# Optimization experiments

Measured on AMD Instinct MI355X. Metric: run time of the kernel, lower is better.

Reference implementation:

```python
import jax, jax.numpy as jnp
import numpy as np

N_DRUG = 572
D = 512
K = 64          # neighbor_sample_size
T = 30000       # tail entities
R = 200         # relations
MAX_DEG = 32    # padded invariant_adj neighbor count
EPS = 1e-5


def setup_inputs() -> dict:
    key = jax.random.key(0)
    ks = jax.random.split(key, 10)
    return {
        "drug_embed_W": jax.random.normal(ks[0], (N_DRUG, D), jnp.float32),
        "rela_embed_W": jax.random.normal(ks[1], (R, D), jnp.float32),
        "ent_embed_W": jax.random.normal(ks[2], (T, D), jnp.float32),
        "Wa": jax.random.normal(ks[3], (D, D), jnp.float32) / np.float32(np.sqrt(D)),
        "lin_W": jax.random.normal(ks[4], (2 * D, D), jnp.float32) / np.float32(np.sqrt(2 * D)),
        "lin_b": jnp.zeros((D,), jnp.float32),
        "gamma": jnp.ones((D,), jnp.float32),
        "beta": jnp.zeros((D,), jnp.float32),
        "drug_name": jnp.arange(N_DRUG, dtype=jnp.int64 if jax.config.jax_enable_x64 else jnp.int32),
        "adj_tail": jax.random.randint(ks[5], (N_DRUG, K), 0, T),
        "adj_relation": jax.random.randint(ks[6], (N_DRUG, K), 0, R),
        "nbr_idx": jax.random.randint(ks[7], (N_DRUG, MAX_DEG), 0, N_DRUG),
        "nbr_deg": jax.random.randint(ks[8], (N_DRUG,), 0, MAX_DEG),
        "epoch": 2,
    }


def _forward(drug_embed_W, rela_embed_W, ent_embed_W, Wa, lin_W, lin_b, gamma, beta,
             drug_name, adj_tail, adj_relation, nbr_idx, nbr_deg, epoch):
    drug_e = drug_embed_W[drug_name]          # [N, D]
    rela = rela_embed_W[adj_relation]         # [N, K, D]
    ent = ent_embed_W[adj_tail]               # [N, K, D]

    # relation-aware attention over sampled neighbors (AttentionLayer)
    q = drug_e @ Wa                           # [N, D]
    scores = jnp.einsum('nd,nkd->nk', q, rela) * (1.0 / np.float32(np.sqrt(D)))
    attn = jax.nn.softmax(scores, axis=1)     # [N, K]
    agg = jnp.einsum('nk,nkd->nd', attn, ent) # [N, D]

    # Linear1: Linear(2D->D) + ReLU + BatchNorm1d (training-mode batch stats)
    h = jnp.concatenate([agg, drug_e], axis=1) @ lin_W + lin_b
    h = jax.nn.relu(h)
    mean = jnp.mean(h, axis=0)
    var = jnp.var(h, axis=0)                  # biased, as torch BN normalization
    drug_f = (h - mean) * jax.lax.rsqrt(var + EPS) * gamma + beta

    if epoch > 1:
        # sequential per-node neighbor-mean smoothing (in-place semantics)
        mask = (jnp.arange(MAX_DEG)[None, :] < nbr_deg[:, None])  # [N, MAX_DEG]

        def step(f, i):
            pos = nbr_idx[i]
            m = mask[i][:, None].astype(f.dtype)
            s = jnp.sum(f[pos] * m, axis=0)
            deg = nbr_deg[i]
            avg = s / jnp.maximum(deg, 1).astype(f.dtype)
            new = jnp.where(deg > 0, (avg + f[i]) * 0.5, f[i])
            return f.at[i].set(new), None

        drug_f, _ = jax.lax.scan(step, drug_f, jnp.arange(N_DRUG))
    return drug_f


def reference(drug_embed_W, rela_embed_W, ent_embed_W, Wa, lin_W, lin_b, gamma, beta,
              drug_name, adj_tail, adj_relation, nbr_idx, nbr_deg, epoch):
    return _forward(drug_embed_W, rela_embed_W, ent_embed_W, Wa, lin_W, lin_b, gamma, beta,
                    drug_name, adj_tail, adj_relation, nbr_idx, nbr_deg, epoch)
```

## Files before the change

kernel.cpp:

```cpp
#include <hip/hip_runtime.h>

#define N_DRUG 572
#define DIM 512
#define MAXDEG 32
#define FS 3

__global__ __launch_bounds__(256) void prep_kernel(
    const float* __restrict__ Wa, const float* __restrict__ relaW,
    const float* __restrict__ linW, float* __restrict__ linP,
    float* __restrict__ relaP)
{
    const int b = blockIdx.x;
    const int t = threadIdx.x;
    if (b < 512) {
        const int g = b * 256 + t;
        const int c = g & 511, k4 = g >> 9;
        const float4 v = make_float4(linW[(size_t)(k4 * 4 + 0) * 512 + c],
                                     linW[(size_t)(k4 * 4 + 1) * 512 + c],
                                     linW[(size_t)(k4 * 4 + 2) * 512 + c],
                                     linW[(size_t)(k4 * 4 + 3) * 512 + c]);
        *(float4*)&linP[((size_t)(c >> 6) * 256 + k4) * 256 + (c & 63) * 4] = v;
        return;
    }
    const int bb = b - 512;
    const int rb = bb >> 5, kb = bb & 31;
    const int wv = t >> 6, l = t & 63;
    const int r0 = rb * 16 + wv * 4;
    const int k0 = kb * 16;

    float a[4][8];
    #pragma unroll
    for (int rr = 0; rr < 4; ++rr) {
        const float4* ap = (const float4*)(relaW + (size_t)min(r0 + rr, 199) * 512 + l * 8);
        const float4 x = ap[0], y = ap[1];
        a[rr][0] = x.x; a[rr][1] = x.y; a[rr][2] = x.z; a[rr][3] = x.w;
        a[rr][4] = y.x; a[rr][5] = y.y; a[rr][6] = y.z; a[rr][7] = y.w;
    }
    float acc[64];
    #pragma unroll
    for (int i = 0; i < 64; ++i) acc[i] = 0.f;
    #pragma unroll
    for (int kk = 0; kk < 16; ++kk) {
        const float4* bp = (const float4*)(Wa + (size_t)(k0 + kk) * 512 + l * 8);
        const float4 x = bp[0], y = bp[1];
        const float bv[8] = {x.x, x.y, x.z, x.w, y.x, y.y, y.z, y.w};
        #pragma unroll
        for (int rr = 0; rr < 4; ++rr) {
            float s = acc[rr * 16 + kk];
            #pragma unroll
            for (int j = 0; j < 8; ++j) s = fmaf(a[rr][j], bv[j], s);
            acc[rr * 16 + kk] = s;
        }
    }
    #pragma unroll
    for (int off = 1; off <= 32; off <<= 1) {
        #pragma unroll
        for (int i = 0; i < 64; ++i) acc[i] += __shfl_xor(acc[i], off, 64);
    }
    float outv = acc[0];
    #pragma unroll
    for (int i = 1; i < 64; ++i) outv = (l == i) ? acc[i] : outv;
    const int rr = l >> 4, kk = l & 15;
    if (r0 + rr < 200) relaP[(size_t)(r0 + rr) * 512 + k0 + kk] = outv;
}

__global__ __launch_bounds__(256) void attn_kernel(
    const float* __restrict__ drugW, const float* __restrict__ relaP,
    const float* __restrict__ entW, const int* __restrict__ dn,
    const int* __restrict__ adj_tail, const int* __restrict__ adj_rel,
    float* __restrict__ cat)
{
    __shared__ float at[64];
    __shared__ int tails[64];
    __shared__ int rels[64];
    const int d = blockIdx.x;
    const int t = threadIdx.x;
    const int w = t >> 6, lane = t & 63;

    if (t < 64) {
        tails[t] = adj_tail[d * 64 + t];
        rels[t]  = adj_rel[d * 64 + t];
    }
    const int rd = dn[d];
    float qv[8];
    {
        const float4* qp = (const float4*)(drugW + (size_t)rd * 512 + lane * 8);
        const float4 x = qp[0], y = qp[1];
        qv[0] = x.x; qv[1] = x.y; qv[2] = x.z; qv[3] = x.w;
        qv[4] = y.x; qv[5] = y.y; qv[6] = y.z; qv[7] = y.w;
    }
    __syncthreads();

    #pragma unroll 4
    for (int kk = 0; kk < 16; ++kk) {
        const int k = w * 16 + kk;
        const float4* p = (const float4*)(relaP + (size_t)rels[k] * 512 + lane * 8);
        const float4 x = p[0], y = p[1];
        float s = 0.f;
        s = fmaf(qv[0], x.x, s); s = fmaf(qv[1], x.y, s);
        s = fmaf(qv[2], x.z, s); s = fmaf(qv[3], x.w, s);
        s = fmaf(qv[4], y.x, s); s = fmaf(qv[5], y.y, s);
        s = fmaf(qv[6], y.z, s); s = fmaf(qv[7], y.w, s);
        #pragma unroll
        for (int off = 32; off >= 1; off >>= 1) s += __shfl_xor(s, off, 64);
        if (lane == 0) at[k] = s * 0.0441941738241592f;
    }
    __syncthreads();

    if (w == 0) {
        const float s = at[lane];
        float m = s;
        #pragma unroll
        for (int off = 32; off >= 1; off >>= 1) m = fmaxf(m, __shfl_xor(m, off, 64));
        const float e = __expf(s - m);
        float sum = e;
        #pragma unroll
        for (int off = 32; off >= 1; off >>= 1) sum += __shfl_xor(sum, off, 64);
        at[lane] = e / sum;
    }
    __syncthreads();

    {
        const int c2 = t * 2;
        float a0 = 0.f, a1 = 0.f;
        #pragma unroll 8
        for (int k = 0; k < 64; ++k) {
            const float ak = at[k];
            const float2 e = *(const float2*)(entW + (size_t)tails[k] * 512 + c2);
            a0 = fmaf(ak, e.x, a0);
            a1 = fmaf(ak, e.y, a1);
        }
        float* o = cat + (size_t)d * 1024;
        *(float2*)&o[c2] = make_float2(a0, a1);
        const float2 de = *(const float2*)(drugW + (size_t)rd * 512 + c2);
        *(float2*)&o[512 + c2] = de;
    }
}

__global__ __launch_bounds__(512) void gemm_h(
    const float* __restrict__ A, const float* __restrict__ linP,
    const float* __restrict__ bias, float* __restrict__ out)
{
    __shared__ float red[8][8][128];
    const int t = threadIdx.x;
    const int wv = t >> 6, lane = t & 63;
    const int r0 = blockIdx.x * 8;
    const int half = lane >> 5;
    const int cw = (lane * 2) & 63;

    const float* wp = linP + ((size_t)(blockIdx.y * 2 + half) * 256 + wv * 32) * 256
                    + cw * 4;
    const float* ap[8];
    #pragma unroll
    for (int r = 0; r < 8; ++r)
        ap[r] = A + (size_t)min(r0 + r, N_DRUG - 1) * 1024 + wv * 128;

    float acc0[8] = {0.f, 0.f, 0.f, 0.f, 0.f, 0.f, 0.f, 0.f};
    float acc1[8] = {0.f, 0.f, 0.f, 0.f, 0.f, 0.f, 0.f, 0.f};
    #pragma unroll 2
    for (int k4 = 0; k4 < 32; ++k4) {
        const float4 w0 = *(const float4*)(wp + (size_t)k4 * 256);
        const float4 w1 = *(const float4*)(wp + (size_t)k4 * 256 + 4);
        #pragma unroll
        for (int r = 0; r < 8; ++r) {
            const float4 a = *(const float4*)(ap[r] + k4 * 4);
            acc0[r] = fmaf(a.x, w0.x, acc0[r]);
            acc0[r] = fmaf(a.y, w0.y, acc0[r]);
            acc0[r] = fmaf(a.z, w0.z, acc0[r]);
            acc0[r] = fmaf(a.w, w0.w, acc0[r]);
            acc1[r] = fmaf(a.x, w1.x, acc1[r]);
            acc1[r] = fmaf(a.y, w1.y, acc1[r]);
            acc1[r] = fmaf(a.z, w1.z, acc1[r]);
            acc1[r] = fmaf(a.w, w1.w, acc1[r]);
        }
    }
    #pragma unroll
    for (int r = 0; r < 8; ++r)
        *(float2*)&red[wv][r][lane * 2] = make_float2(acc0[r], acc1[r]);
    __syncthreads();

    #pragma unroll
    for (int u = 0; u < 2; ++u) {
        const int o = u * 512 + t;
        const int r = o >> 7, cc = o & 127;
        if (r0 + r < N_DRUG) {
            float v = red[0][r][cc];
            #pragma unroll
            for (int w = 1; w < 8; ++w) v += red[w][r][cc];
            v += bias[blockIdx.y * 128 + cc];
            out[(size_t)(r0 + r) * 512 + blockIdx.y * 128 + cc] = fmaxf(v, 0.f);
        }
    }
}

__global__ __launch_bounds__(64) void scan_kernel(
    float* hout, const float* __restrict__ gamma, const float* __restrict__ beta,
    const int* __restrict__ nbr_idx, const int* __restrict__ nbr_deg,
    const int* __restrict__ epoch)
{
    __shared__ float fs[(N_DRUG + 1) * FS];
    __shared__ alignas(16) unsigned short offs[N_DRUG * MAXDEG];
    __shared__ float2 ivw[N_DRUG];
    __shared__ int   mxs[N_DRUG];

    const int lane = threadIdx.x;
    const int col  = lane & 1;
    const int rg   = lane >> 1;
    const int c0   = blockIdx.x * 2;

    for (int i = lane; i < N_DRUG; i += 64) {
        const int d = nbr_deg[i];
        ivw[i] = (d > 0) ? make_float2(0.5f / (float)d, 0.5f) : make_float2(0.f, 1.f);
        const int4* np = (const int4*)&nbr_idx[i * MAXDEG];
        uint2* op = (uint2*)&offs[i * MAXDEG];
        int mx = -1;
        #pragma unroll
        for (int u = 0; u < 8; ++u) {
            int4 qq = np[u];
            const int b = u * 4;
            qq.x = (b + 0 < d) ? qq.x : N_DRUG;
            qq.y = (b + 1 < d) ? qq.y : N_DRUG;
            qq.z = (b + 2 < d) ? qq.z : N_DRUG;
            qq.w = (b + 3 < d) ? qq.w : N_DRUG;
            mx = max(mx, (qq.x < i) ? qq.x : -1);
            mx = max(mx, (qq.y < i) ? qq.y : -1);
            mx = max(mx, (qq.z < i) ? qq.z : -1);
            mx = max(mx, (qq.w < i) ? qq.w : -1);
            op[u] = make_uint2((unsigned)(qq.x * FS) | ((unsigned)(qq.y * FS) << 16),
                               (unsigned)(qq.z * FS) | ((unsigned)(qq.w * FS) << 16));
        }
        mxs[i] = mx;
    }

    float sl = 0.f, ql = 0.f;
    for (int r = rg; r < N_DRUG; r += 32) {
        const float v = hout[(size_t)r * DIM + c0 + col];
        fs[r * FS + col] = v;
        sl += v;
        ql = fmaf(v, v, ql);
    }
    if (lane < FS) fs[N_DRUG * FS + lane] = 0.f;
    #pragma unroll
    for (int off = 2; off <= 32; off <<= 1) {
        sl += __shfl_xor(sl, off, 64);
        ql += __shfl_xor(ql, off, 64);
    }
    const float mean = sl * (1.f / N_DRUG);
    const float var  = ql * (1.f / N_DRUG) - mean * mean;
    const float rstd = rsqrtf(var + 1e-5f);
    const float scl  = gamma[c0 + col] * rstd;
    const float shf  = beta[c0 + col] - mean * scl;

    for (int r = rg; r < N_DRUG; r += 32)
        fs[r * FS + col] = fmaf(fs[r * FS + col], scl, shf);

    if (epoch[0] > 1) {
        const int j  = lane >> 2;
        const int hh = (lane >> 1) & 1;
        const int cl = lane & 1;

        int gs = 0;
        int ge;
        {
            const int jj = 1 + lane;
            const bool flag = (lane >= 15) || (jj >= N_DRUG) ||
                              (mxs[min(jj, N_DRUG - 1)] >= 0);
            ge = 1 + (int)__builtin_ctzll(__ballot(flag) & 0xFFFFULL);
        }
        uint4 ca, cb;
        {
            const uint4* p = (const uint4*)&offs[j * MAXDEG + hh * 16];
            ca = p[0]; cb = p[1];
        }
        while (gs < N_DRUG) {
            const bool pred = (gs + j) < ge;
            float s0 = 0.f, s1 = 0.f;
#define G2(W) { s0 += fs[(W & 0xffffu) + cl]; s1 += fs[(W >> 16) + cl]; }
            if (pred) { G2(ca.x) G2(ca.y) G2(ca.z) G2(ca.w)
                        G2(cb.x) G2(cb.y) G2(cb.z) G2(cb.w) }
#undef G2
            uint4 na, nb;
            {
                const uint4* p = (const uint4*)&offs[min(ge + j, N_DRUG - 1) * MAXDEG + hh * 16];
                na = p[0]; nb = p[1];
            }
            int genext;
            {
                const int jj = ge + 1 + lane;
                const bool flag = (lane >= 15) || (jj >= N_DRUG) ||
                                  (mxs[min(jj, N_DRUG - 1)] >= ge);
                genext = ge + 1 + (int)__builtin_ctzll(__ballot(flag) & 0xFFFFULL);
            }
            float nv = 0.f;
            if (pred) {
                const float cur = fs[(gs + j) * FS + cl];
                const float2 iw = ivw[gs + j];
                float sh = s0 + s1;
                sh += __shfl_xor(sh, 2, 64);
                nv = fmaf(sh, iw.x, cur * iw.y);
            }
            asm volatile("" ::: "memory");
            if (pred && hh == 0) fs[(gs + j) * FS + cl] = nv;
            asm volatile("" ::: "memory");
            gs = ge;
            ge = genext;
            ca = na; cb = nb;
        }
    }

    for (int r = rg; r < N_DRUG; r += 32)
        hout[(size_t)r * DIM + c0 + col] = fs[r * FS + col];
}

extern "C" void kernel_launch(void* const* d_in, const int* in_sizes, int n_in,
                              void* d_out, int out_size, void* d_ws, size_t ws_size,
                              hipStream_t stream)
{
    const float* drugW = (const float*)d_in[0];
    const float* relaW = (const float*)d_in[1];
    const float* entW  = (const float*)d_in[2];
    const float* Wa    = (const float*)d_in[3];
    const float* linW  = (const float*)d_in[4];
    const float* linb  = (const float*)d_in[5];
    const float* gamma = (const float*)d_in[6];
    const float* beta  = (const float*)d_in[7];
    const int* drug_name = (const int*)d_in[8];
    const int* adj_tail  = (const int*)d_in[9];
    const int* adj_rel   = (const int*)d_in[10];
    const int* nbr_idx   = (const int*)d_in[11];
    const int* nbr_deg   = (const int*)d_in[12];
    const int* epoch     = (const int*)d_in[13];

    float* out = (float*)d_out;

    float* linP  = (float*)d_ws;
    float* relaP = (float*)((char*)d_ws + 2097152);
    float* cat   = (float*)((char*)d_ws + 2506752);

    prep_kernel<<<928, 256, 0, stream>>>(Wa, relaW, linW, linP, relaP);
    attn_kernel<<<N_DRUG, 256, 0, stream>>>(drugW, relaP, entW, drug_name,
                                            adj_tail, adj_rel, cat);
    gemm_h<<<dim3(72, 4), 512, 0, stream>>>(cat, linP, linb, out);
    scan_kernel<<<256, 64, 0, stream>>>(out, gamma, beta, nbr_idx, nbr_deg, epoch);
}
```

Before: 232.2 us.

## Precompute wavefront schedule once in prep kernel and prefetch scan state

The dependency-group schedule for the sequential neighbor smoothing is now computed once by an extra block of the prep kernel and written to workspace. Previously each of the 256 scan blocks recomputed it with a ballot on the serial critical path. The scan loop now reads the next group boundaries from shared memory, prefetches the next row's current value and weights, and replaces the cross-lane shuffle with a DPP move. Byte-offset tables are duplicated per column to drop an add from address computation, at the cost of extra shared memory.

```diff
diff --git a/kernel.cpp b/kernel.cpp
--- a/kernel.cpp
+++ b/kernel.cpp
@@ -3,12 +3,13 @@
 #define N_DRUG 572
 #define DIM 512
 #define MAXDEG 32
-#define FS 3
+#define FSB 12
 
 __global__ __launch_bounds__(256) void prep_kernel(
     const float* __restrict__ Wa, const float* __restrict__ relaW,
-    const float* __restrict__ linW, float* __restrict__ linP,
-    float* __restrict__ relaP)
+    const float* __restrict__ linW, const int* __restrict__ nbr_idx,
+    const int* __restrict__ nbr_deg, float* __restrict__ linP,
+    float* __restrict__ relaP, int* __restrict__ sched_g)
 {
     const int b = blockIdx.x;
     const int t = threadIdx.x;
@@ -22,6 +23,44 @@
         *(float4*)&linP[((size_t)(c >> 6) * 256 + k4) * 256 + (c & 63) * 4] = v;
         return;
     }
+    if (b == 928) {
+        __shared__ int mxs2[N_DRUG];
+        for (int i = t; i < N_DRUG; i += 256) {
+            const int d = nbr_deg[i];
+            const int4* np = (const int4*)&nbr_idx[i * MAXDEG];
+            int mx = -1;
+            #pragma unroll
+            for (int u = 0; u < 8; ++u) {
+                const int4 qq = np[u];
+                const int bb = u * 4;
+                mx = max(mx, (bb + 0 < d && qq.x < i) ? qq.x : -1);
+                mx = max(mx, (bb + 1 < d && qq.y < i) ? qq.y : -1);
+                mx = max(mx, (bb + 2 < d && qq.z < i) ? qq.z : -1);
+                mx = max(mx, (bb + 3 < d && qq.w < i) ? qq.w : -1);
+            }
+            mxs2[i] = mx;
+        }
+        __syncthreads();
+        if (t < 64) {
+            int gs = 0, nr = 0;
+            if (t == 0) sched_g[0] = 0;
+            while (gs < N_DRUG) {
+                const int jj = gs + 1 + t;
+                const bool flag = (t >= 15) || (jj >= N_DRUG) ||
+                                  (mxs2[min(jj, N_DRUG - 1)] >= gs);
+                const int ge = gs + 1 + (int)__builtin_ctzll(__ballot(flag) & 0xFFFFULL);
+                ++nr;
+                if (t == 0) sched_g[nr] = ge;
+                gs = ge;
+            }
+            if (t == 0) {
+                sched_g[nr + 1] = N_DRUG;
+                sched_g[nr + 2] = N_DRUG;
+                sched_g[nr + 3] = N_DRUG;
+            }
+        }
+        return;
+    }
     const int bb = b - 512;
     const int rb = bb >> 5, kb = bb & 31;
     const int wv = t >> 6, l = t & 63;
@@ -196,50 +235,51 @@
 __global__ __launch_bounds__(64) void scan_kernel(
     float* hout, const float* __restrict__ gamma, const float* __restrict__ beta,
     const int* __restrict__ nbr_idx, const int* __restrict__ nbr_deg,
-    const int* __restrict__ epoch)
-{
-    __shared__ float fs[(N_DRUG + 1) * FS];
-    __shared__ alignas(16) unsigned short offs[N_DRUG * MAXDEG];
+    const int* __restrict__ epoch, const int* __restrict__ sched_g)
+{
+    __shared__ alignas(16) unsigned char fsb[(N_DRUG + 1) * FSB];
+    __shared__ alignas(16) unsigned short offsA[N_DRUG * MAXDEG];
+    __shared__ alignas(16) unsigned short offsB[N_DRUG * MAXDEG];
     __shared__ float2 ivw[N_DRUG];
-    __shared__ int   mxs[N_DRUG];
+    __shared__ int sched[N_DRUG + 8];
 
     const int lane = threadIdx.x;
     const int col  = lane & 1;
     const int rg   = lane >> 1;
     const int c0   = blockIdx.x * 2;
+    const int cl4  = col * 4;
+
+    for (int i = lane; i < N_DRUG + 8; i += 64) sched[i] = sched_g[i];
 
     for (int i = lane; i < N_DRUG; i += 64) {
         const int d = nbr_deg[i];
         ivw[i] = (d > 0) ? make_float2(0.5f / (float)d, 0.5f) : make_float2(0.f, 1.f);
         const int4* np = (const int4*)&nbr_idx[i * MAXDEG];
-        uint2* op = (uint2*)&offs[i * MAXDEG];
-        int mx = -1;
+        uint2* opA = (uint2*)&offsA[i * MAXDEG];
+        uint2* opB = (uint2*)&offsB[i * MAXDEG];
         #pragma unroll
         for (int u = 0; u < 8; ++u) {
-            int4 qq = np[u];
+            const int4 qq = np[u];
             const int b = u * 4;
-            qq.x = (b + 0 < d) ? qq.x : N_DRUG;
-            qq.y = (b + 1 < d) ? qq.y : N_DRUG;
-            qq.z = (b + 2 < d) ? qq.z : N_DRUG;
-            qq.w = (b + 3 < d) ? qq.w : N_DRUG;
-            mx = max(mx, (qq.x < i) ? qq.x : -1);
-            mx = max(mx, (qq.y < i) ? qq.y : -1);
-            mx = max(mx, (qq.z < i) ? qq.z : -1);
-            mx = max(mx, (qq.w < i) ? qq.w : -1);
-            op[u] = make_uint2((unsigned)(qq.x * FS) | ((unsigned)(qq.y * FS) << 16),
-                               (unsigned)(qq.z * FS) | ((unsigned)(qq.w * FS) << 16));
-        }
-        mxs[i] = mx;
+            const int rx = (b + 0 < d) ? qq.x : N_DRUG;
+            const int ry = (b + 1 < d) ? qq.y : N_DRUG;
+            const int rz = (b + 2 < d) ? qq.z : N_DRUG;
+            const int rw = (b + 3 < d) ? qq.w : N_DRUG;
+            const unsigned w0 = (unsigned)(rx * FSB) | ((unsigned)(ry * FSB) << 16);
+            const unsigned w1 = (unsigned)(rz * FSB) | ((unsigned)(rw * FSB) << 16);
+            opA[u] = make_uint2(w0, w1);
+            opB[u] = make_uint2(w0 + 0x00040004u, w1 + 0x00040004u);
+        }
     }
 
     float sl = 0.f, ql = 0.f;
     for (int r = rg; r < N_DRUG; r += 32) {
         const float v = hout[(size_t)r * DIM + c0 + col];
-        fs[r * FS + col] = v;
+        *(float*)(fsb + r * FSB + cl4) = v;
         sl += v;
         ql = fmaf(v, v, ql);
     }
-    if (lane < FS) fs[N_DRUG * FS + lane] = 0.f;
+    if (lane < 3) *(float*)(fsb + N_DRUG * FSB + lane * 4) = 0.f;
     #pragma unroll
     for (int off = 2; off <= 32; off <<= 1) {
         sl += __shfl_xor(sl, off, 64);
@@ -251,65 +291,64 @@
     const float scl  = gamma[c0 + col] * rstd;
     const float shf  = beta[c0 + col] - mean * scl;
 
-    for (int r = rg; r < N_DRUG; r += 32)
-        fs[r * FS + col] = fmaf(fs[r * FS + col], scl, shf);
+    for (int r = rg; r < N_DRUG; r += 32) {
+        float* p = (float*)(fsb + r * FSB + cl4);
+        *p = fmaf(*p, scl, shf);
+    }
 
     if (epoch[0] > 1) {
         const int j  = lane >> 2;
         const int hh = (lane >> 1) & 1;
-        const int cl = lane & 1;
-
-        int gs = 0;
-        int ge;
-        {
-            const int jj = 1 + lane;
-            const bool flag = (lane >= 15) || (jj >= N_DRUG) ||
-                              (mxs[min(jj, N_DRUG - 1)] >= 0);
-            ge = 1 + (int)__builtin_ctzll(__ballot(flag) & 0xFFFFULL);
-        }
+        const unsigned short* obase = col ? offsB : offsA;
+
+        int gs  = 0;
+        int ge  = sched[1];
+        int ge2 = sched[2];
+        int rp  = 3;
         uint4 ca, cb;
         {
-            const uint4* p = (const uint4*)&offs[j * MAXDEG + hh * 16];
+            const uint4* p = (const uint4*)&obase[j * MAXDEG + hh * 16];
             ca = p[0]; cb = p[1];
         }
+        float  cur = *(const float*)(fsb + j * FSB + cl4);
+        float2 iw  = ivw[j];
+
         while (gs < N_DRUG) {
             const bool pred = (gs + j) < ge;
             float s0 = 0.f, s1 = 0.f;
-#define G2(W) { s0 += fs[(W & 0xffffu) + cl]; s1 += fs[(W >> 16) + cl]; }
-            if (pred) { G2(ca.x) G2(ca.y) G2(ca.z) G2(ca.w)
-                        G2(cb.x) G2(cb.y) G2(cb.z) G2(cb.w) }
+            if (pred) {
+#define G2(W) { s0 += *(const float*)(fsb + (W & 0xffffu)); \
+                s1 += *(const float*)(fsb + (W >> 16)); }
+                G2(ca.x) G2(ca.y) G2(ca.z) G2(ca.w)
+                G2(cb.x) G2(cb.y) G2(cb.z) G2(cb.w)
 #undef G2
+            }
             uint4 na, nb;
             {
-                const uint4* p = (const uint4*)&offs[min(ge + j, N_DRUG - 1) * MAXDEG + hh * 16];
+                const uint4* p = (const uint4*)&obase[min(ge + j, N_DRUG - 1) * MAXDEG + hh * 16];
                 na = p[0]; nb = p[1];
             }
-            int genext;
-            {
-                const int jj = ge + 1 + lane;
-                const bool flag = (lane >= 15) || (jj >= N_DRUG) ||
-                                  (mxs[min(jj, N_DRUG - 1)] >= ge);
-                genext = ge + 1 + (int)__builtin_ctzll(__ballot(flag) & 0xFFFFULL);
-            }
+            const float  ncur = *(const float*)(fsb + min(ge + j, N_DRUG) * FSB + cl4);
+            const float2 niw  = ivw[min(ge + j, N_DRUG - 1)];
+            const int    nge  = sched[rp];
+
             float nv = 0.f;
             if (pred) {
-                const float cur = fs[(gs + j) * FS + cl];
-                const float2 iw = ivw[gs + j];
                 float sh = s0 + s1;
-                sh += __shfl_xor(sh, 2, 64);
+                sh += __int_as_float(__builtin_amdgcn_mov_dpp(
+                          __float_as_int(sh), 0x4E, 0xF, 0xF, false));
                 nv = fmaf(sh, iw.x, cur * iw.y);
             }
             asm volatile("" ::: "memory");
-            if (pred && hh == 0) fs[(gs + j) * FS + cl] = nv;
+            if (pred && hh == 0) *(float*)(fsb + (gs + j) * FSB + cl4) = nv;
             asm volatile("" ::: "memory");
-            gs = ge;
-            ge = genext;
-            ca = na; cb = nb;
+            gs = ge; ge = ge2; ge2 = nge; ++rp;
+            ca = na; cb = nb; cur = ncur; iw = niw;
         }
     }
 
     for (int r = rg; r < N_DRUG; r += 32)
-        hout[(size_t)r * DIM + c0 + col] = fs[r * FS + col];
+        hout[(size_t)r * DIM + c0 + col] = *(const float*)(fsb + r * FSB + cl4);
 }
 
 extern "C" void kernel_launch(void* const* d_in, const int* in_sizes, int n_in,
@@ -333,13 +372,16 @@
 
     float* out = (float*)d_out;
 
-    float* linP  = (float*)d_ws;
-    float* relaP = (float*)((char*)d_ws + 2097152);
-    float* cat   = (float*)((char*)d_ws + 2506752);
-
-    prep_kernel<<<928, 256, 0, stream>>>(Wa, relaW, linW, linP, relaP);
+    float* linP   = (float*)d_ws;
+    float* relaP  = (float*)((char*)d_ws + 2097152);
+    float* cat    = (float*)((char*)d_ws + 2506752);
+    int*   sched  = (int*)  ((char*)d_ws + 4849664);
+
+    prep_kernel<<<929, 256, 0, stream>>>(Wa, relaW, linW, nbr_idx, nbr_deg,
+                                         linP, relaP, sched);
     attn_kernel<<<N_DRUG, 256, 0, stream>>>(drugW, relaP, entW, drug_name,
                                             adj_tail, adj_rel, cat);
     gemm_h<<<dim3(72, 4), 512, 0, stream>>>(cat, linP, linb, out);
-    scan_kernel<<<256, 64, 0, stream>>>(out, gamma, beta, nbr_idx, nbr_deg, epoch);
-}
+    scan_kernel<<<256, 64, 0, stream>>>(out, gamma, beta, nbr_idx, nbr_deg,
+                                        epoch, sched);
+}
```

Measured after the change: 224.0 us. -3.5%, faster.
